# Optimization experiments

Measured on AMD Instinct MI355X. Metric: run time of the kernel, lower is better.

Reference implementation:

```python
import jax, jax.numpy as jnp
import numpy as np

B, T, IN, H, OUT = 64, 1024, 64, 512, 64


def setup_inputs() -> dict:
    key = jax.random.key(0)
    ks = jax.random.split(key, 11)
    s = 0.05  # small init to avoid gate saturation
    return {
        "x": jax.random.normal(ks[0], (B, T, IN), jnp.float32),
        "W_ih1": jax.random.normal(ks[1], (4 * H, IN), jnp.float32) * s,
        "W_hh1": jax.random.normal(ks[2], (4 * H, H), jnp.float32) * s,
        "b_ih1": jax.random.normal(ks[3], (4 * H,), jnp.float32) * s,
        "b_hh1": jax.random.normal(ks[4], (4 * H,), jnp.float32) * s,
        "W_ih2": jax.random.normal(ks[5], (4 * H, H), jnp.float32) * s,
        "W_hh2": jax.random.normal(ks[6], (4 * H, H), jnp.float32) * s,
        "b_ih2": jax.random.normal(ks[7], (4 * H,), jnp.float32) * s,
        "b_hh2": jax.random.normal(ks[8], (4 * H,), jnp.float32) * s,
        "W_out": jax.random.normal(ks[9], (OUT, H), jnp.float32) * s,
        "b_out": jax.random.normal(ks[10], (OUT,), jnp.float32) * s,
    }


def _lstm_cell(x_t, h, c, W_ih, W_hh, b_ih, b_hh):
    # PyTorch LSTMCell: gates ordered i, f, g, o
    gates = x_t @ W_ih.T + b_ih + h @ W_hh.T + b_hh  # [B, 4H]
    i, f, g, o = jnp.split(gates, 4, axis=-1)
    i = jax.nn.sigmoid(i)
    f = jax.nn.sigmoid(f)
    g = jnp.tanh(g)
    o = jax.nn.sigmoid(o)
    c_new = f * c + i * g
    h_new = o * jnp.tanh(c_new)
    return h_new, c_new


def reference(x, W_ih1, W_hh1, b_ih1, b_hh1, W_ih2, W_hh2, b_ih2, b_hh2,
              W_out, b_out):
    batch = x.shape[0]
    h1 = jnp.zeros((batch, W_hh1.shape[1]), x.dtype)
    c1 = jnp.zeros_like(h1)
    h2 = jnp.zeros((batch, W_hh2.shape[1]), x.dtype)
    c2 = jnp.zeros_like(h2)

    def step(carry, x_t):
        h1, c1, h2, c2 = carry
        h1, c1 = _lstm_cell(x_t, h1, c1, W_ih1, W_hh1, b_ih1, b_hh1)
        h2, c2 = _lstm_cell(h1, h2, c2, W_ih2, W_hh2, b_ih2, b_hh2)
        y_t = h2 @ W_out.T + b_out  # per-step Linear head
        return (h1, c1, h2, c2), y_t

    xs = jnp.swapaxes(x, 0, 1)  # [T, B, IN]
    _, ys = jax.lax.scan(step, (h1, c1, h2, c2), xs)
    return jnp.swapaxes(ys, 0, 1)  # [B, T, OUT]
```

## Files before the change

### kernel.cpp

```cpp
#include <hip/hip_runtime.h>

#define B_    64
#define T_    1024
#define IN_   64
#define H_    512
#define OUT_  64
#define SLOTS 8
#define NWG   130
#define NWORD 6144

typedef _Float16 f16;
typedef _Float16 half8 __attribute__((ext_vector_type(8)));
typedef float    floatx4 __attribute__((ext_vector_type(4)));
typedef unsigned int u32;
typedef unsigned short u16;
typedef unsigned long long u64;

#define MFMA16(a,b,c) __builtin_amdgcn_mfma_f32_16x16x32_f16((a),(b),(c),0,0,0)

#define XS_OFF   0
#define HB_OFF   8192
#define CC_OFF   9216
#define RED_OFF  11264
#define H1W_OFF  44032
#define H2W_OFF  101376

__device__ __forceinline__ float sigmoidf_(float x) {
    return 1.0f / (1.0f + __expf(-x));
}
__device__ __forceinline__ float tanhf_(float x) {
    float ax = fabsf(x);
    float e  = __expf(-2.0f * ax);
    float t  = (1.0f - e) / (1.0f + e);
    return x >= 0.0f ? t : -t;
}

__device__ __forceinline__ u32 flag_peek(const u32* p) {
    return __hip_atomic_load(p, __ATOMIC_RELAXED, __HIP_MEMORY_SCOPE_AGENT);
}
__device__ __forceinline__ void wait_ge(u32* p, u32 v) {
    while (__hip_atomic_load(p, __ATOMIC_RELAXED, __HIP_MEMORY_SCOPE_AGENT) < v)
        __builtin_amdgcn_s_sleep(1);
}
__device__ __forceinline__ void flag_add(u32* p) {
    __hip_atomic_fetch_add(p, 1u, __ATOMIC_RELAXED, __HIP_MEMORY_SCOPE_AGENT);
}
__device__ __forceinline__ void astore8w(u64* p, u64 v) {
    __hip_atomic_store(p, v, __ATOMIC_RELAXED, __HIP_MEMORY_SCOPE_SYSTEM);
}
__device__ __forceinline__ u64 aload8w(const u64* p) {
    return __hip_atomic_load(p, __ATOMIC_RELAXED, __HIP_MEMORY_SCOPE_SYSTEM);
}

__device__ __forceinline__ void stage_poll(char* smem, int ldsOff, const u64* g,
                                           u32 exp, int tid, const int* soff) {
    u32 pend = 0xFFFu;
    do {
        u64 vv[12];
        #pragma unroll
        for (int i = 0; i < 12; ++i)
            vv[i] = aload8w(g + i*512 + tid);
        #pragma unroll
        for (int i = 0; i < 12; ++i) {
            if ((pend & (1u << i)) && (u32)(vv[i] >> 48) == exp) {
                *(u64*)(smem + ldsOff + soff[i]) = vv[i];
                pend &= ~(1u << i);
            }
        }
        if (pend) __builtin_amdgcn_s_sleep(1);
    } while (pend);
}

__device__ __forceinline__ half8 frag_pk(const char* p) {
    const u64* q = (const u64*)p;
    u64 w0 = q[0], w1 = q[1], w2 = q[2];
    u32 b = (u32)(w0 >> 32), c = (u32)w1, d = (u32)(w1 >> 32);
    union { u32 u[4]; half8 h; } U;
    U.u[0] = (u32)w0;
    U.u[1] = (b & 0xffffu) | (c << 16);
    U.u[2] = (c >> 16) | (d << 16);
    U.u[3] = (u32)w2;
    return U.h;
}
#define WB(jt,row,wi) (((jt)*224 + (row)*7 + (wi)) * 8)

__global__ void pack_w1(const float* __restrict__ Wih, const float* __restrict__ Whh,
                        f16* __restrict__ Wp) {
    int idx = blockIdx.x * 256 + threadIdx.x;
    if (idx >= 4*32*18*512) return;
    int j    = idx & 7;
    int lane = (idx >> 3) & 63;
    int kt   = (idx >> 9) % 18;
    int r    = (idx >> 9) / 18;
    int jt   = r & 31;
    int g    = r >> 5;
    int n = g*512 + jt*16 + (lane & 15);
    int k = kt*32 + (lane >> 4)*8 + j;
    float v = (k < 64) ? Wih[n*64 + k] : Whh[n*512 + (k - 64)];
    Wp[idx] = (f16)v;
}

__global__ void pack_w2(const float* __restrict__ Wih, const float* __restrict__ Whh,
                        f16* __restrict__ Wp) {
    int idx = blockIdx.x * 256 + threadIdx.x;
    if (idx >= 4*32*32*512) return;
    int j    = idx & 7;
    int lane = (idx >> 3) & 63;
    int kt   = (idx >> 9) & 31;
    int r    = idx >> 14;
    int jt   = r & 31;
    int g    = r >> 5;
    int n = g*512 + jt*16 + (lane & 15);
    int k = kt*32 + (lane >> 4)*8 + j;
    float v = (k < 512) ? Wih[n*512 + k] : Whh[n*512 + (k - 512)];
    Wp[idx] = (f16)v;
}

__global__ void pack_wo(const float* __restrict__ Wout, f16* __restrict__ Wp) {
    int idx = blockIdx.x * 256 + threadIdx.x;
    if (idx >= 4*16*512) return;
    int j    = idx & 7;
    int lane = (idx >> 3) & 63;
    int kt   = (idx >> 9) & 15;
    int nt   = idx >> 13;
    int n = nt*16 + (lane & 15);
    int k = kt*32 + (lane >> 4)*8 + j;
    Wp[idx] = (f16)Wout[n*512 + k];
}

__global__ void bias_sum(const float* __restrict__ a1, const float* __restrict__ b1,
                         const float* __restrict__ a2, const float* __restrict__ b2,
                         float* __restrict__ s1, float* __restrict__ s2) {
    int i = blockIdx.x * 256 + threadIdx.x;
    if (i >= 2048) return;
    s1[i] = a1[i] + b1[i];
    s2[i] = a2[i] + b2[i];
}

__global__ __launch_bounds__(512, 1) void lstm_persist(
    const float* __restrict__ x,
    const f16*  __restrict__ W1p,
    const f16*  __restrict__ W2p,
    const f16*  __restrict__ Wop,
    const float* __restrict__ bs1,
    const float* __restrict__ bs2,
    const float* __restrict__ bout,
    u64*  __restrict__ h1w,
    u64*  __restrict__ h2w,
    float* __restrict__ y,
    u32*  __restrict__ arr2,
    u32*  __restrict__ arrH)
{
    __shared__ __align__(16) char smem[158720];
    float* RED = (float*)(smem + RED_OFF);
    float* CC  = (float*)(smem + CC_OFF);

    const int wg   = blockIdx.x;
    const int tid  = threadIdx.x;
    const int lane = tid & 63;
    const int w    = tid >> 6;
    const int col  = lane & 15;
    const int quad = lane >> 4;

    int soff[12];
    #pragma unroll
    for (int i = 0; i < 12; ++i) {
        const int ww = i*512 + tid;
        const int jt_ = ww / 192, rr = ww - jt_*192;
        soff[i] = WB(jt_, rr/6, rr%6);
    }
    const int pr  = tid / 6, pi = tid - pr*6;
    const int pj  = pi % 3;
    const int pc0 = pr*16 + (pi/3)*8 + pj*3;
    const u16* hb = (const u16*)(smem + HB_OFF);

    if (wg < 64) {
        const int jt = wg & 31, bhalf = wg >> 5;
        const int gp = w & 1, kq = w >> 1;
        half8 wrx[2];
        half8 wrh[2][4];
        if (kq < 2) {
            #pragma unroll
            for (int gi = 0; gi < 2; ++gi)
                wrx[gi] = *(const half8*)(W1p + ((size_t)(((gp*2+gi)*32 + jt)*18 + kq)*64 + lane)*8);
        }
        #pragma unroll
        for (int gi = 0; gi < 2; ++gi)
            #pragma unroll
            for (int k = 0; k < 4; ++k) {
                const int kt = 2 + kq*4 + k;
                wrh[gi][k] = *(const half8*)(W1p + ((size_t)(((gp*2+gi)*32 + jt)*18 + kt)*64 + lane)*8);
            }
        float bsr[4];
        #pragma unroll
        for (int g = 0; g < 4; ++g) bsr[g] = bs1[g*512 + jt*16 + (tid & 15)];
        CC[tid] = 0.f;

        u32* a2 = arr2 + bhalf*1024;
        const int lbx = tid >> 4, kcx = tid & 15;
        const float* xbase = x + (size_t)(bhalf*32 + lbx)*T_*(size_t)IN_ + ((kcx ^ (lbx & 7)) * 4);

        *(float4*)(smem + XS_OFF + tid*16) = *(const float4*)xbase;
        stage_poll(smem, H1W_OFF, h1w + (size_t)(7*2 + bhalf)*NWORD, 0u, tid, soff);
        __syncthreads();

        for (int t = 0; t < T_; ++t) {
            float4 xreg;
            if (t + 1 < T_) xreg = *(const float4*)(xbase + (size_t)(t+1)*IN_);

            floatx4 acc[2][2] = {{{0.f,0.f,0.f,0.f},{0.f,0.f,0.f,0.f}},
                                 {{0.f,0.f,0.f,0.f},{0.f,0.f,0.f,0.f}}};
            #pragma unroll
            for (int m = 0; m < 2; ++m) {
                const int lb_a = m*16 + col, sw = lb_a & 7;
                if (kq < 2) {
                    const int fg = kq*8 + quad*2;
                    float4 u = *(const float4*)(smem + XS_OFF + ((size_t)lb_a*16 + (fg ^ sw))*16);
                    float4 v = *(const float4*)(smem + XS_OFF + ((size_t)lb_a*16 + ((fg+1) ^ sw))*16);
                    half8 a = (half8){(f16)u.x,(f16)u.y,(f16)u.z,(f16)u.w,
                                      (f16)v.x,(f16)v.y,(f16)v.z,(f16)v.w};
                    acc[0][m] = MFMA16(a, wrx[0], acc[0][m]);
                    acc[1][m] = MFMA16(a, wrx[1], acc[1][m]);
                }
                #pragma unroll
                for (int k = 0; k < 4; ++k) {
                    const int kc = kq*16 + k*4 + quad;
                    half8 a = frag_pk(smem + H1W_OFF + WB(kc>>1, lb_a, (kc&1)*3));
                    acc[0][m] = MFMA16(a, wrh[0][k], acc[0][m]);
                    acc[1][m] = MFMA16(a, wrh[1][k], acc[1][m]);
                }
            }
            #pragma unroll
            for (int gi = 0; gi < 2; ++gi) {
                const int g = gp*2 + gi;
                #pragma unroll
                for (int m = 0; m < 2; ++m)
                    #pragma unroll
                    for (int r = 0; r < 4; ++r)
                        RED[kq*2048 + g*512 + (m*16 + quad*4 + r)*16 + col] = acc[gi][m][r];
            }
            __syncthreads();
            {
                float gt[4];
                #pragma unroll
                for (int g = 0; g < 4; ++g)
                    gt[g] = RED[       g*512 + tid] + RED[2048 + g*512 + tid]
                          + RED[4096 + g*512 + tid] + RED[6144 + g*512 + tid] + bsr[g];
                const float i_ = sigmoidf_(gt[0]);
                const float f_ = sigmoidf_(gt[1]);
                const float g_ = tanhf_(gt[2]);
                const float o_ = sigmoidf_(gt[3]);
                const float cn = f_ * CC[tid] + i_ * g_;
                CC[tid] = cn;
                ((f16*)(smem + HB_OFF))[tid] = (f16)(o_ * tanhf_(cn));
            }
            __syncthreads();
            if (tid < 192) {
                u64 wv = (u64)hb[pc0] | ((u64)hb[pc0+1] << 16)
                       | ((pj < 2) ? ((u64)hb[pc0+2] << 32) : 0)
                       | ((u64)(u32)(t + 1) << 48);
                astore8w(h1w + (size_t)((t & 7)*2 + bhalf)*NWORD + jt*192 + tid, wv);
            }
            const bool needA2 = (tid == 0) && (t + 1 < T_) && (t + 1 >= SLOTS);
            u32 fA2 = needA2 ? flag_peek(a2 + (t + 1 - SLOTS)) : 32u;
            if (t + 1 < T_) {
                *(float4*)(smem + XS_OFF + tid*16) = xreg;
                stage_poll(smem, H1W_OFF, h1w + (size_t)((t & 7)*2 + bhalf)*NWORD,
                           (u32)(t + 1), tid, soff);
            }
            if (needA2 && fA2 < 32u) wait_ge(a2 + (t + 1 - SLOTS), 32u);
            __syncthreads();
        }
    } else if (wg < 128) {
        const int v = wg - 64;
        const int jt = v & 31, bhalf = v >> 5;
        const int gp = w & 1, kq = w >> 1;
        half8 wrA[2][4], wrB[2][4];
        #pragma unroll
        for (int gi = 0; gi < 2; ++gi)
            #pragma unroll
            for (int k = 0; k < 4; ++k) {
                const int ktA = kq*4 + k;
                const int ktB = 16 + kq*4 + k;
                wrA[gi][k] = *(const half8*)(W2p + ((size_t)(((gp*2+gi)*32 + jt)*32 + ktA)*64 + lane)*8);
                wrB[gi][k] = *(const half8*)(W2p + ((size_t)(((gp*2+gi)*32 + jt)*32 + ktB)*64 + lane)*8);
            }
        float bsr[4];
        #pragma unroll
        for (int g = 0; g < 4; ++g) bsr[g] = bs2[g*512 + jt*16 + (tid & 15)];
        CC[tid] = 0.f;

        u32* a2 = arr2 + bhalf*1024;
        u32* aH = arrH + bhalf*1024;

        stage_poll(smem, H1W_OFF, h1w + (size_t)(0*2 + bhalf)*NWORD, 1u, tid, soff);
        stage_poll(smem, H2W_OFF, h2w + (size_t)(7*2 + bhalf)*NWORD, 0u, tid, soff);
        __syncthreads();

        for (int t2 = 0; t2 < T_; ++t2) {
            floatx4 acc[2][2] = {{{0.f,0.f,0.f,0.f},{0.f,0.f,0.f,0.f}},
                                 {{0.f,0.f,0.f,0.f},{0.f,0.f,0.f,0.f}}};
            #pragma unroll
            for (int m = 0; m < 2; ++m) {
                const int lb_a = m*16 + col;
                #pragma unroll
                for (int k = 0; k < 4; ++k) {
                    const int kc = kq*16 + k*4 + quad;
                    half8 a = frag_pk(smem + H1W_OFF + WB(kc>>1, lb_a, (kc&1)*3));
                    acc[0][m] = MFMA16(a, wrA[0][k], acc[0][m]);
                    acc[1][m] = MFMA16(a, wrA[1][k], acc[1][m]);
                }
            }
            #pragma unroll
            for (int m = 0; m < 2; ++m) {
                const int lb_a = m*16 + col;
                #pragma unroll
                for (int k = 0; k < 4; ++k) {
                    const int kc = kq*16 + k*4 + quad;
                    half8 a = frag_pk(smem + H2W_OFF + WB(kc>>1, lb_a, (kc&1)*3));
                    acc[0][m] = MFMA16(a, wrB[0][k], acc[0][m]);
                    acc[1][m] = MFMA16(a, wrB[1][k], acc[1][m]);
                }
            }
            #pragma unroll
            for (int gi = 0; gi < 2; ++gi) {
                const int g = gp*2 + gi;
                #pragma unroll
                for (int m = 0; m < 2; ++m)
                    #pragma unroll
                    for (int r = 0; r < 4; ++r)
                        RED[kq*2048 + g*512 + (m*16 + quad*4 + r)*16 + col] = acc[gi][m][r];
            }
            __syncthreads();
            {
                float gt[4];
                #pragma unroll
                for (int g = 0; g < 4; ++g)
                    gt[g] = RED[       g*512 + tid] + RED[2048 + g*512 + tid]
                          + RED[4096 + g*512 + tid] + RED[6144 + g*512 + tid] + bsr[g];
                const float i_ = sigmoidf_(gt[0]);
                const float f_ = sigmoidf_(gt[1]);
                const float g_ = tanhf_(gt[2]);
                const float o_ = sigmoidf_(gt[3]);
                const float cn = f_ * CC[tid] + i_ * g_;
                CC[tid] = cn;
                ((f16*)(smem + HB_OFF))[tid] = (f16)(o_ * tanhf_(cn));
            }
            __syncthreads();
            if (tid < 192) {
                u64 wv = (u64)hb[pc0] | ((u64)hb[pc0+1] << 16)
                       | ((pj < 2) ? ((u64)hb[pc0+2] << 32) : 0)
                       | ((u64)(u32)(t2 + 1) << 48);
                astore8w(h2w + (size_t)((t2 & 7)*2 + bhalf)*NWORD + jt*192 + tid, wv);
            }
            if (tid == 0) flag_add(a2 + t2);
            const bool needAH = (tid == 0) && (t2 + 1 < T_) && (t2 + 1 >= SLOTS);
            u32 fAH = needAH ? flag_peek(aH + (t2 + 1 - SLOTS)) : 1u;
            if (t2 + 1 < T_) {
                stage_poll(smem, H1W_OFF, h1w + (size_t)(((t2+1) & 7)*2 + bhalf)*NWORD,
                           (u32)(t2 + 2), tid, soff);
                stage_poll(smem, H2W_OFF, h2w + (size_t)((t2 & 7)*2 + bhalf)*NWORD,
                           (u32)(t2 + 1), tid, soff);
            }
            if (needAH && fAH < 1u) wait_ge(aH + (t2 + 1 - SLOTS), 1u);
            __syncthreads();
        }
    } else {
        const int bhalf = wg - 128;
        const int nt = w & 3, kh = w >> 2;
        half8 wr[8];
        #pragma unroll
        for (int k = 0; k < 8; ++k) {
            const int kt = kh*8 + k;
            wr[k] = *(const half8*)(Wop + ((size_t)(nt*16 + kt)*64 + lane)*8);
        }
        const float boutr = bout[nt*16 + col];
        u32* aH = arrH + bhalf*1024;
        const int lb0 = col, lb1 = 16 + col;

        stage_poll(smem, H1W_OFF, h2w + (size_t)(0*2 + bhalf)*NWORD, 1u, tid, soff);
        __syncthreads();
        if (tid == 0) flag_add(aH + 0);

        for (int t3 = 0; t3 < T_; ++t3) {
            floatx4 acc0 = {0.f,0.f,0.f,0.f}, acc1 = {0.f,0.f,0.f,0.f};
            #pragma unroll
            for (int k = 0; k < 8; ++k) {
                const int kc = (kh*8 + k)*4 + quad;
                half8 a0  = frag_pk(smem + H1W_OFF + WB(kc>>1, lb0, (kc&1)*3));
                half8 a1v = frag_pk(smem + H1W_OFF + WB(kc>>1, lb1, (kc&1)*3));
                acc0 = MFMA16(a0,  wr[k], acc0);
                acc1 = MFMA16(a1v, wr[k], acc1);
            }
            if (kh == 1) {
                #pragma unroll
                for (int r = 0; r < 4; ++r) {
                    RED[(nt*2+0)*256 + (quad*4 + r)*16 + col] = acc0[r];
                    RED[(nt*2+1)*256 + (quad*4 + r)*16 + col] = acc1[r];
                }
            }
            __syncthreads();
            if (kh == 0) {
                #pragma unroll
                for (int r = 0; r < 4; ++r) {
                    const float v0 = acc0[r] + RED[(nt*2+0)*256 + (quad*4 + r)*16 + col] + boutr;
                    const float v1 = acc1[r] + RED[(nt*2+1)*256 + (quad*4 + r)*16 + col] + boutr;
                    const int b0 = bhalf*32 +  0 + quad*4 + r;
                    const int b1 = bhalf*32 + 16 + quad*4 + r;
                    y[((size_t)b0*T_ + t3)*OUT_ + nt*16 + col] = v0;
                    y[((size_t)b1*T_ + t3)*OUT_ + nt*16 + col] = v1;
                }
            }
            __syncthreads();
            if (t3 + 1 < T_) {
                stage_poll(smem, H1W_OFF, h2w + (size_t)(((t3+1) & 7)*2 + bhalf)*NWORD,
                           (u32)(t3 + 2), tid, soff);
                __syncthreads();
                if (tid == 0) flag_add(aH + (t3 + 1));
            }
        }
    }
}

extern "C" void kernel_launch(void* const* d_in, const int* in_sizes, int n_in,
                              void* d_out, int out_size, void* d_ws, size_t ws_size,
                              hipStream_t stream) {
    const float* x    = (const float*)d_in[0];
    const float* Wih1 = (const float*)d_in[1];
    const float* Whh1 = (const float*)d_in[2];
    const float* bih1 = (const float*)d_in[3];
    const float* bhh1 = (const float*)d_in[4];
    const float* Wih2 = (const float*)d_in[5];
    const float* Whh2 = (const float*)d_in[6];
    const float* bih2 = (const float*)d_in[7];
    const float* bhh2 = (const float*)d_in[8];
    const float* Wout = (const float*)d_in[9];
    const float* bout = (const float*)d_in[10];
    float* y = (float*)d_out;

    char* ws = (char*)d_ws;
    f16*   W1p   = (f16*)(ws + 0);
    f16*   W2p   = (f16*)(ws + 2359296);
    f16*   Wop   = (f16*)(ws + 6553600);
    float* bs1   = (float*)(ws + 6619136);
    float* bs2   = (float*)(ws + 6627328);
    u64*   h1w   = (u64*)(ws + 6635520);
    u64*   h2w   = (u64*)(ws + 7421952);
    u32*   arr2  = (u32*)(ws + 8208384);
    u32*   arrH  = (u32*)(ws + 8216576);

    hipMemsetAsync(ws + 6635520, 0, 1589248, stream);

    pack_w1<<<4608, 256, 0, stream>>>(Wih1, Whh1, W1p);
    pack_w2<<<8192, 256, 0, stream>>>(Wih2, Whh2, W2p);
    pack_wo<<<128, 256, 0, stream>>>(Wout, Wop);
    bias_sum<<<8, 256, 0, stream>>>(bih1, bhh1, bih2, bhh2, bs1, bs2);

    lstm_persist<<<NWG, 512, 0, stream>>>(x, W1p, W2p, Wop, bs1, bs2, bout,
                                          h1w, h2w, y, arr2, arrH);
}
```

Measured before the change: 4.786 ms.

## Assign recurrence roles by XCD so each ring exchanges hidden state via agent-scope L2

The kernel launches 256 workgroups, reads each workgroup's XCC hardware register, and uses atomics to claim 130 roles so that each group of 32 cooperating workgroups for a batch-half/layer lands on one XCD. Surplus workgroups exit. When a ring is confirmed co-resident, hidden-state words are also written to and polled from a separate ring buffer with agent-scope atomics instead of system-scope ones. The aim is to keep the per-step exchange in the shared L2 rather than going through slower coherent memory. A timeout falls back to the system-scope buffer. This adds startup claim logic, extra stores and a larger workspace memset, and depends on the assumption that agent scope behaves coherently within a single XCD.

```diff
diff --git a/kernel.cpp b/kernel.cpp
--- a/kernel.cpp
+++ b/kernel.cpp
@@ -6,8 +6,10 @@
 #define H_    512
 #define OUT_  64
 #define SLOTS 8
-#define NWG   130
+#define NWG   256
+#define NROLE 130
 #define NWORD 6144
+#define RSLOT (8*NWORD)
 
 typedef _Float16 f16;
 typedef _Float16 half8 __attribute__((ext_vector_type(8)));
@@ -51,6 +53,12 @@
 __device__ __forceinline__ u64 aload8w(const u64* p) {
     return __hip_atomic_load(p, __ATOMIC_RELAXED, __HIP_MEMORY_SCOPE_SYSTEM);
 }
+__device__ __forceinline__ void astore8a(u64* p, u64 v) {
+    __hip_atomic_store(p, v, __ATOMIC_RELAXED, __HIP_MEMORY_SCOPE_AGENT);
+}
+__device__ __forceinline__ u64 aload8a(const u64* p) {
+    return __hip_atomic_load(p, __ATOMIC_RELAXED, __HIP_MEMORY_SCOPE_AGENT);
+}
 
 __device__ __forceinline__ void stage_poll(char* smem, int ldsOff, const u64* g,
                                            u32 exp, int tid, const int* soff) {
@@ -68,6 +76,36 @@
             }
         }
         if (pend) __builtin_amdgcn_s_sleep(1);
+    } while (pend);
+}
+
+__device__ __forceinline__ void stage_poll_r(char* smem, int ldsOff,
+                                             const u64* gr, const u64* gs,
+                                             u32 exp, int tid, const int* soff,
+                                             int coh, int* esc) {
+    u32 pend = 0xFFFu;
+    int rounds = 0;
+    bool useSys = (!coh) || (*esc != 0);
+    do {
+        u64 vv[12];
+        if (!useSys) {
+            #pragma unroll
+            for (int i = 0; i < 12; ++i) vv[i] = aload8a(gr + i*512 + tid);
+        } else {
+            #pragma unroll
+            for (int i = 0; i < 12; ++i) vv[i] = aload8w(gs + i*512 + tid);
+        }
+        #pragma unroll
+        for (int i = 0; i < 12; ++i) {
+            if ((pend & (1u << i)) && (u32)(vv[i] >> 48) == exp) {
+                *(u64*)(smem + ldsOff + soff[i]) = vv[i];
+                pend &= ~(1u << i);
+            }
+        }
+        if (pend) {
+            __builtin_amdgcn_s_sleep(1);
+            if (!useSys && ++rounds >= 1024) { useSys = true; *esc = 1; }
+        }
     } while (pend);
 }
 
@@ -147,20 +185,82 @@
     const float* __restrict__ bout,
     u64*  __restrict__ h1w,
     u64*  __restrict__ h2w,
+    u64*  __restrict__ hring,
     float* __restrict__ y,
     u32*  __restrict__ arr2,
-    u32*  __restrict__ arrH)
+    u32*  __restrict__ arrH,
+    u32*  __restrict__ ctrl)
 {
     __shared__ __align__(16) char smem[158720];
+    __shared__ int s_role, s_coh;
     float* RED = (float*)(smem + RED_OFF);
     float* CC  = (float*)(smem + CC_OFF);
 
-    const int wg   = blockIdx.x;
     const int tid  = threadIdx.x;
     const int lane = tid & 63;
     const int w    = tid >> 6;
     const int col  = lane & 15;
     const int quad = lane >> 4;
+
+    u32 xcd;
+    asm volatile("s_getreg_b32 %0, hwreg(HW_REG_XCC_ID)" : "=s"(xcd));
+    xcd &= 7u;
+    if (tid == 0) {
+        u32* cnt     = ctrl;
+        u32* claimed = ctrl + 8;
+        u32* taken   = ctrl + 16;
+        u32* mx      = ctrl + 160;
+        u32* rcnt    = ctrl + 288;
+        int role = -1;
+        u32 rank = __hip_atomic_fetch_add(&cnt[xcd], 1u, __ATOMIC_RELAXED, __HIP_MEMORY_SCOPE_AGENT);
+        int pref = -1;
+        if (xcd < 4u)       { if (rank < 32u) pref = (int)(xcd*32u + rank); }
+        else if (xcd == 4u) { if (rank < 2u)  pref = 128 + (int)rank; }
+        if (pref >= 0) {
+            u32 e0 = 0;
+            if (__hip_atomic_compare_exchange_strong(&taken[pref], &e0, 1u,
+                    __ATOMIC_RELAXED, __ATOMIC_RELAXED, __HIP_MEMORY_SCOPE_AGENT))
+                role = pref;
+        }
+        if (role < 0) {
+            if (pref < 0)
+                for (int s = 0; s < 100; ++s) __builtin_amdgcn_s_sleep(64);
+            while (role < 0) {
+                if (__hip_atomic_load(claimed, __ATOMIC_RELAXED, __HIP_MEMORY_SCOPE_AGENT) >= (u32)NROLE)
+                    break;
+                for (int r = 0; r < NROLE; ++r) {
+                    u32 e0 = 0;
+                    if (__hip_atomic_load(&taken[r], __ATOMIC_RELAXED, __HIP_MEMORY_SCOPE_AGENT) == 0u &&
+                        __hip_atomic_compare_exchange_strong(&taken[r], &e0, 1u,
+                            __ATOMIC_RELAXED, __ATOMIC_RELAXED, __HIP_MEMORY_SCOPE_AGENT)) {
+                        role = r; break;
+                    }
+                }
+            }
+        }
+        int coh = 0;
+        if (role >= 0) {
+            __hip_atomic_fetch_add(claimed, 1u, __ATOMIC_RELAXED, __HIP_MEMORY_SCOPE_AGENT);
+            if (role < 128) {
+                const int ring = role >> 5;
+                __hip_atomic_store(&mx[role], xcd + 1u, __ATOMIC_RELAXED, __HIP_MEMORY_SCOPE_AGENT);
+                __hip_atomic_fetch_add(&rcnt[ring], 1u, __ATOMIC_RELEASE, __HIP_MEMORY_SCOPE_AGENT);
+                while (__hip_atomic_load(&rcnt[ring], __ATOMIC_ACQUIRE, __HIP_MEMORY_SCOPE_AGENT) < 32u)
+                    __builtin_amdgcn_s_sleep(1);
+                coh = 1;
+                u32 x0 = __hip_atomic_load(&mx[ring*32], __ATOMIC_RELAXED, __HIP_MEMORY_SCOPE_AGENT);
+                for (int i = 1; i < 32; ++i)
+                    if (__hip_atomic_load(&mx[ring*32 + i], __ATOMIC_RELAXED, __HIP_MEMORY_SCOPE_AGENT) != x0)
+                        coh = 0;
+            }
+        }
+        s_role = role;
+        s_coh  = coh;
+    }
+    __syncthreads();
+    const int role = s_role;
+    const int coh  = s_coh;
+    if (role < 0) return;
 
     int soff[12];
     #pragma unroll
@@ -174,8 +274,11 @@
     const int pc0 = pr*16 + (pi/3)*8 + pj*3;
     const u16* hb = (const u16*)(smem + HB_OFF);
 
-    if (wg < 64) {
-        const int jt = wg & 31, bhalf = wg >> 5;
+    if (role < 64) {
+        const int bhalf = role >> 5, jt = role & 31;
+        u64* rbuf = hring + (size_t)bhalf * RSLOT;
+        int* esc  = (int*)(smem + H2W_OFF);
+        if (tid == 0) *esc = 0;
         const int gp = w & 1, kq = w >> 1;
         half8 wrx[2];
         half8 wrh[2][4];
@@ -201,7 +304,9 @@
         const float* xbase = x + (size_t)(bhalf*32 + lbx)*T_*(size_t)IN_ + ((kcx ^ (lbx & 7)) * 4);
 
         *(float4*)(smem + XS_OFF + tid*16) = *(const float4*)xbase;
-        stage_poll(smem, H1W_OFF, h1w + (size_t)(7*2 + bhalf)*NWORD, 0u, tid, soff);
+        __syncthreads();
+        stage_poll_r(smem, H1W_OFF, rbuf + (size_t)7*NWORD,
+                     h1w + (size_t)(7*2 + bhalf)*NWORD, 0u, tid, soff, coh, esc);
         __syncthreads();
 
         for (int t = 0; t < T_; ++t) {
@@ -260,20 +365,25 @@
                        | ((pj < 2) ? ((u64)hb[pc0+2] << 32) : 0)
                        | ((u64)(u32)(t + 1) << 48);
                 astore8w(h1w + (size_t)((t & 7)*2 + bhalf)*NWORD + jt*192 + tid, wv);
+                if (coh) astore8a(rbuf + (size_t)(t & 7)*NWORD + jt*192 + tid, wv);
             }
             const bool needA2 = (tid == 0) && (t + 1 < T_) && (t + 1 >= SLOTS);
             u32 fA2 = needA2 ? flag_peek(a2 + (t + 1 - SLOTS)) : 32u;
             if (t + 1 < T_) {
                 *(float4*)(smem + XS_OFF + tid*16) = xreg;
-                stage_poll(smem, H1W_OFF, h1w + (size_t)((t & 7)*2 + bhalf)*NWORD,
-                           (u32)(t + 1), tid, soff);
+                stage_poll_r(smem, H1W_OFF, rbuf + (size_t)(t & 7)*NWORD,
+                             h1w + (size_t)((t & 7)*2 + bhalf)*NWORD,
+                             (u32)(t + 1), tid, soff, coh, esc);
             }
             if (needA2 && fA2 < 32u) wait_ge(a2 + (t + 1 - SLOTS), 32u);
             __syncthreads();
         }
-    } else if (wg < 128) {
-        const int v = wg - 64;
-        const int jt = v & 31, bhalf = v >> 5;
+    } else if (role < 128) {
+        const int v = role - 64;
+        const int bhalf = v >> 5, jt = v & 31;
+        u64* rbuf = hring + (size_t)(2 + bhalf) * RSLOT;
+        int* esc  = (int*)(smem + XS_OFF);
+        if (tid == 0) *esc = 0;
         const int gp = w & 1, kq = w >> 1;
         half8 wrA[2][4], wrB[2][4];
         #pragma unroll
@@ -293,8 +403,10 @@
         u32* a2 = arr2 + bhalf*1024;
         u32* aH = arrH + bhalf*1024;
 
+        __syncthreads();
         stage_poll(smem, H1W_OFF, h1w + (size_t)(0*2 + bhalf)*NWORD, 1u, tid, soff);
-        stage_poll(smem, H2W_OFF, h2w + (size_t)(7*2 + bhalf)*NWORD, 0u, tid, soff);
+        stage_poll_r(smem, H2W_OFF, rbuf + (size_t)7*NWORD,
+                     h2w + (size_t)(7*2 + bhalf)*NWORD, 0u, tid, soff, coh, esc);
         __syncthreads();
 
         for (int t2 = 0; t2 < T_; ++t2) {
@@ -352,6 +464,7 @@
                        | ((pj < 2) ? ((u64)hb[pc0+2] << 32) : 0)
                        | ((u64)(u32)(t2 + 1) << 48);
                 astore8w(h2w + (size_t)((t2 & 7)*2 + bhalf)*NWORD + jt*192 + tid, wv);
+                if (coh) astore8a(rbuf + (size_t)(t2 & 7)*NWORD + jt*192 + tid, wv);
             }
             if (tid == 0) flag_add(a2 + t2);
             const bool needAH = (tid == 0) && (t2 + 1 < T_) && (t2 + 1 >= SLOTS);
@@ -359,14 +472,15 @@
             if (t2 + 1 < T_) {
                 stage_poll(smem, H1W_OFF, h1w + (size_t)(((t2+1) & 7)*2 + bhalf)*NWORD,
                            (u32)(t2 + 2), tid, soff);
-                stage_poll(smem, H2W_OFF, h2w + (size_t)((t2 & 7)*2 + bhalf)*NWORD,
-                           (u32)(t2 + 1), tid, soff);
+                stage_poll_r(smem, H2W_OFF, rbuf + (size_t)(t2 & 7)*NWORD,
+                             h2w + (size_t)((t2 & 7)*2 + bhalf)*NWORD,
+                             (u32)(t2 + 1), tid, soff, coh, esc);
             }
             if (needAH && fAH < 1u) wait_ge(aH + (t2 + 1 - SLOTS), 1u);
             __syncthreads();
         }
     } else {
-        const int bhalf = wg - 128;
+        const int bhalf = role - 128;
         const int nt = w & 3, kh = w >> 2;
         half8 wr[8];
         #pragma unroll
@@ -448,8 +562,10 @@
     u64*   h2w   = (u64*)(ws + 7421952);
     u32*   arr2  = (u32*)(ws + 8208384);
     u32*   arrH  = (u32*)(ws + 8216576);
-
-    hipMemsetAsync(ws + 6635520, 0, 1589248, stream);
+    u64*   hring = (u64*)(ws + 8224768);
+    u32*   ctrl  = (u32*)(ws + 9797632);
+
+    hipMemsetAsync(ws + 6635520, 0, 3163280, stream);
 
     pack_w1<<<4608, 256, 0, stream>>>(Wih1, Whh1, W1p);
     pack_w2<<<8192, 256, 0, stream>>>(Wih2, Whh2, W2p);
@@ -457,5 +573,5 @@
     bias_sum<<<8, 256, 0, stream>>>(bih1, bhh1, bih2, bhh2, bs1, bs2);
 
     lstm_persist<<<NWG, 512, 0, stream>>>(x, W1p, W2p, Wop, bs1, bs2, bout,
-                                          h1w, h2w, y, arr2, arrH);
-}
+                                          h1w, h2w, hring, y, arr2, arrH, ctrl);
+}
```

After: 4.373 ms. 8.6% less time.
